# Kernel tuning notes

Measured on AMD Instinct MI355X. Metric: run time of the kernel, lower is better.

The kernel has to match this reference:

```python
import jax, jax.numpy as jnp
import numpy as np

B, LQ, H, NH, LK, N = 32, 256, 256, 8, 512, 8192
DH = H // NH
EPS = 1e-12

def layer_norm(x, g, b):
    m = x.mean(-1, keepdims=True)
    v = ((x - m) ** 2).mean(-1, keepdims=True)
    return (x - m) / jnp.sqrt(v + EPS) * g + b

def setup_inputs() -> dict:
    rs = np.random.RandomState(0)
    counts = rs.randint(LK // 2, LK + 1, size=B)  # ragged per-graph edge counts, max = LK
    E = int(counts.sum())
    edge_batch = jnp.asarray(np.repeat(np.arange(B), counts), jnp.int32)
    edge_pos = jnp.asarray(np.concatenate([np.arange(c) for c in counts]), jnp.int32)
    pad_mask = jnp.asarray((np.arange(LK)[None, :] < counts[:, None]).astype(np.float32))
    src = jnp.asarray(rs.randint(0, N, E), jnp.int32)
    dst = jnp.asarray(rs.randint(0, N, E), jnp.int32)
    ks = jax.random.split(jax.random.key(0), 16)
    def rn(i, shape, s=0.02):
        return jax.random.normal(ks[i], shape, jnp.float32) * s
    return dict(
        extended_attention_mask=jnp.zeros((B, 1, 1, LQ), jnp.float32),
        query=rn(0, (B, LQ, H), 1.0),
        rel_embedding_output=rn(1, (E, H), 1.0),
        graph_output=rn(2, (N, H), 1.0),
        src=src, dst=dst, edge_batch=edge_batch, edge_pos=edge_pos, pad_mask=pad_mask,
        Wq=rn(3, (H, H)), bq=jnp.zeros((H,), jnp.float32),
        Wk=rn(4, (2 * H, H)), bk=jnp.zeros((H,), jnp.float32),
        Wv=rn(5, (H, H)), bv=jnp.zeros((H,), jnp.float32),
        Wo=rn(6, (H, H)), bo=jnp.zeros((H,), jnp.float32),
        ln1_g=jnp.ones((H,), jnp.float32), ln1_b=jnp.zeros((H,), jnp.float32),
        W1=rn(7, (H, H)), b1=jnp.zeros((H,), jnp.float32),
        W2=rn(8, (H, H)), b2=jnp.zeros((H,), jnp.float32),
        ln2_g=jnp.ones((H,), jnp.float32), ln2_b=jnp.zeros((H,), jnp.float32),
    )

def reference(extended_attention_mask, query, rel_embedding_output, graph_output,
              src, dst, edge_batch, edge_pos, pad_mask,
              Wq, bq, Wk, bk, Wv, bv, Wo, bo, ln1_g, ln1_b,
              W1, b1, W2, b2, ln2_g, ln2_b):
    # --- memory_transform: edge gather + ragged pad (vectorized scatter) ---
    key_flat = jnp.concatenate([graph_output[src], rel_embedding_output], -1)  # [E, 2H]
    dst_flat = graph_output[dst]                                               # [E, H]
    key_pad = jnp.zeros((B, LK, 2 * H), key_flat.dtype).at[edge_batch, edge_pos].set(key_flat)
    val_pad = jnp.zeros((B, LK, H), dst_flat.dtype).at[edge_batch, edge_pos].set(dst_flat)
    cross_mask = (1.0 - pad_mask)[:, None, None, :] * -10000.0                 # [B,1,1,LK]
    # --- BidiAttention ---
    Q = (query @ Wq + bq).reshape(B, LQ, NH, DH)
    K = (key_pad @ Wk + bk).reshape(B, LK, NH, DH)
    V = (val_pad @ Wv + bv).reshape(B, LK, NH, DH)
    scores = jnp.einsum('bqhd,bkhd->bhqk', Q, K) / np.float32(np.sqrt(DH))
    pq = jax.nn.softmax(scores + cross_mask, axis=-1)
    query_ctx = jnp.einsum('bhqk,bkhd->bqhd', pq, V).reshape(B, LQ, H)
    pv = jax.nn.softmax(scores.transpose(0, 1, 3, 2) + extended_attention_mask, axis=-1)
    value_ctx = jnp.einsum('bhkq,bqhd->bkhd', pv, Q).reshape(B, LK, H)
    # --- RelAwareCross output / gate ---
    query_out = layer_norm(query_ctx @ Wo + bo + query, ln1_g, ln1_b)
    theta = jax.nn.sigmoid(value_ctx @ W1 + b1 + val_pad @ W2 + b2)
    value_new = layer_norm(theta * value_ctx + (1.0 - theta) * val_pad, ln2_g, ln2_b)
    # --- memory_update: unpad + scatter-mean by dst, replace rows with incoming edges ---
    val_edges = value_new[edge_batch, edge_pos]                                # [E, H]
    sums = jax.ops.segment_sum(val_edges, dst, num_segments=N)
    cnts = jax.ops.segment_sum(jnp.ones((val_edges.shape[0],), val_edges.dtype), dst, num_segments=N)
    mean = sums / jnp.maximum(cnts, 1.0)[:, None]
    graph_new = jnp.where((cnts > 0)[:, None], mean, graph_output)
    return (graph_new, query_out)
```

## Files before the change

### kernel.cpp

```cpp
#include <hip/hip_runtime.h>
#include <hip/hip_bf16.h>
#include <string.h>

#define B_ 32
#define LQ_ 256
#define H_ 256
#define NH_ 8
#define LK_ 512
#define N_ 8192
#define DH_ 32

typedef float floatx4 __attribute__((ext_vector_type(4)));
typedef short shortx8 __attribute__((ext_vector_type(8)));
typedef short shortx4 __attribute__((ext_vector_type(4)));

__device__ __forceinline__ short f2b(float f) {
    __hip_bfloat16 h = __float2bfloat16(f);
    short s;
    __builtin_memcpy(&s, &h, 2);
    return s;
}
__device__ __forceinline__ float b2f(short s) {
    unsigned u = ((unsigned)(unsigned short)s) << 16;
    float f;
    __builtin_memcpy(&f, &u, 4);
    return f;
}

#define LOG2E 1.44269504088896f

__global__ __launch_bounds__(256) void phase1(
    const float* __restrict__ graph, const float* __restrict__ rel,
    const int* __restrict__ src, const int* __restrict__ dst,
    const int* __restrict__ eb, const int* __restrict__ ep,
    const float* __restrict__ pad_mask,
    const float* __restrict__ Wq, const float* __restrict__ Wk,
    const float* __restrict__ Wv, const float* __restrict__ Wo,
    const float* __restrict__ W1, const float* __restrict__ W2,
    short* __restrict__ WT, short* __restrict__ key_pad,
    short* __restrict__ val_pad, int* __restrict__ head,
    int* __restrict__ row2e, int E) {
    const int bid = blockIdx.x, tid = threadIdx.x;
    if (bid < 8192) {
        int row = bid * 2 + (tid >> 7);
        int t = tid & 127;
        int b = row >> 9, p = row & 511;
        bool valid = pad_mask[row] > 0.5f;
        size_t krow = (size_t)row * 512;
        size_t vrow = (size_t)row * 256;
        int kc = t * 4, vc = t * 2;
        if (valid) {
            int lo = 0, hi = E;
            while (lo < hi) { int mid = (lo + hi) >> 1; if (eb[mid] < b) lo = mid + 1; else hi = mid; }
            int e = lo + p;
            int s = src[e], d = dst[e];
            const float* sp = (kc < 256) ? (graph + (size_t)s * 256 + kc)
                                         : (rel + (size_t)e * 256 + (kc - 256));
            float4 k4 = *(const float4*)sp;
            key_pad[krow + kc + 0] = f2b(k4.x);
            key_pad[krow + kc + 1] = f2b(k4.y);
            key_pad[krow + kc + 2] = f2b(k4.z);
            key_pad[krow + kc + 3] = f2b(k4.w);
            float2 v2 = *(const float2*)(graph + (size_t)d * 256 + vc);
            val_pad[vrow + vc + 0] = f2b(v2.x);
            val_pad[vrow + vc + 1] = f2b(v2.y);
        } else {
            *(long long*)&key_pad[krow + kc] = 0;
            *(int*)&val_pad[vrow + vc] = 0;
        }
    } else if (bid < 9984) {
        int i = (bid - 8192) * 256 + tid;
        const float* s;
        int K, loc;
        if (i < 65536) { s = Wq; K = 256; loc = i; }
        else if (i < 196608) { s = Wk; K = 512; loc = i - 65536; }
        else {
            int m = (i - 196608) >> 16;
            loc = (i - 196608) & 65535;
            K = 256;
            s = (m == 0) ? Wv : (m == 1) ? Wo : (m == 2) ? W1 : W2;
        }
        int n = loc / K, k = loc - n * K;
        WT[i] = f2b(s[(size_t)k * 256 + n]);
    } else {
        int i = (bid - 9984) * 256 + tid;
        if (i < 8192) head[i] = -1;
        for (int j = i; j < E; j += 8192)
            row2e[eb[j] * 512 + ep[j]] = j;
    }
}

__global__ __launch_bounds__(256) void phase2_gemm(
    const float* __restrict__ query, const short* __restrict__ key_pad,
    const short* __restrict__ val_pad, const short* __restrict__ WT,
    const float* __restrict__ bq, const float* __restrict__ bk,
    const float* __restrict__ bv,
    short* __restrict__ Qb, short* __restrict__ Kb,
    short* __restrict__ Vt, short* __restrict__ Qt) {
    __shared__ short As[128][40];
    __shared__ short Bs[128][40];
    const int tid = threadIdx.x;
    const int id = blockIdx.x;
    const float* Af = nullptr; const short* Ab = nullptr;
    const float* Bf = nullptr; const short* Bb = nullptr;
    const float* bias; short* C;
    size_t cbase; int cstride, K; bool biasM;
    if (id < 128) {
        int mt = id >> 1, nt = id & 1;
        Af = query + (size_t)(mt * 128) * 256; K = 256;
        Bb = WT + (size_t)(nt * 128) * 256;
        bias = bq + nt * 128; biasM = false;
        C = Qb; cbase = (size_t)(mt * 128) * 256 + nt * 128; cstride = 256;
    } else if (id < 384) {
        int t = id - 128; int mt = t >> 1, nt = t & 1;
        Ab = key_pad + (size_t)(mt * 128) * 512; K = 512;
        Bb = WT + 65536 + (size_t)(nt * 128) * 512;
        bias = bk + nt * 128; biasM = false;
        C = Kb; cbase = (size_t)(mt * 128) * 256 + nt * 128; cstride = 256;
    } else if (id < 640) {
        int t = id - 384; int b = t >> 3, ct = (t >> 2) & 1, nt = t & 3;
        Ab = WT + 196608 + (size_t)(ct * 128) * 256; K = 256;
        Bb = val_pad + ((size_t)(b * 512 + nt * 128)) * 256;
        bias = bv + ct * 128; biasM = true;
        C = Vt; cbase = ((size_t)(b * 256 + ct * 128)) * 512 + nt * 128; cstride = 512;
    } else {
        int t = id - 640; int b = t >> 2, ct = (t >> 1) & 1, qt = t & 1;
        Ab = WT + (size_t)(ct * 128) * 256; K = 256;
        Bf = query + ((size_t)(b * 256 + qt * 128)) * 256;
        bias = bq + ct * 128; biasM = true;
        C = Qt; cbase = ((size_t)(b * 256 + ct * 128)) * 256 + qt * 128; cstride = 256;
    }
    const int w = tid >> 6, lane = tid & 63;
    const int R0 = (w >> 1) * 64, C0 = (w & 1) * 64;
    const int lm = lane & 15, quad = lane >> 4;
    const int sr = tid >> 1, skq = (tid & 1) * 16;

    floatx4 acc[4][4];
#pragma unroll
    for (int i = 0; i < 4; i++)
#pragma unroll
        for (int j = 0; j < 4; j++) acc[i][j] = {0.f, 0.f, 0.f, 0.f};

    for (int kc = 0; kc < K; kc += 32) {
        if (Af) {
            const float* ap = Af + (size_t)sr * K + kc + skq;
            float4 a1 = *(const float4*)ap, a2 = *(const float4*)(ap + 4);
            float4 a3 = *(const float4*)(ap + 8), a4 = *(const float4*)(ap + 12);
            As[sr][skq + 0] = f2b(a1.x); As[sr][skq + 1] = f2b(a1.y);
            As[sr][skq + 2] = f2b(a1.z); As[sr][skq + 3] = f2b(a1.w);
            As[sr][skq + 4] = f2b(a2.x); As[sr][skq + 5] = f2b(a2.y);
            As[sr][skq + 6] = f2b(a2.z); As[sr][skq + 7] = f2b(a2.w);
            As[sr][skq + 8] = f2b(a3.x); As[sr][skq + 9] = f2b(a3.y);
            As[sr][skq + 10] = f2b(a3.z); As[sr][skq + 11] = f2b(a3.w);
            As[sr][skq + 12] = f2b(a4.x); As[sr][skq + 13] = f2b(a4.y);
            As[sr][skq + 14] = f2b(a4.z); As[sr][skq + 15] = f2b(a4.w);
        } else {
            const short* ap = Ab + (size_t)sr * K + kc + skq;
            *(shortx8*)&As[sr][skq] = *(const shortx8*)ap;
            *(shortx8*)&As[sr][skq + 8] = *(const shortx8*)(ap + 8);
        }
        if (Bf) {
            const float* bp = Bf + (size_t)sr * K + kc + skq;
            float4 a1 = *(const float4*)bp, a2 = *(const float4*)(bp + 4);
            float4 a3 = *(const float4*)(bp + 8), a4 = *(const float4*)(bp + 12);
            Bs[sr][skq + 0] = f2b(a1.x); Bs[sr][skq + 1] = f2b(a1.y);
            Bs[sr][skq + 2] = f2b(a1.z); Bs[sr][skq + 3] = f2b(a1.w);
            Bs[sr][skq + 4] = f2b(a2.x); Bs[sr][skq + 5] = f2b(a2.y);
            Bs[sr][skq + 6] = f2b(a2.z); Bs[sr][skq + 7] = f2b(a2.w);
            Bs[sr][skq + 8] = f2b(a3.x); Bs[sr][skq + 9] = f2b(a3.y);
            Bs[sr][skq + 10] = f2b(a3.z); Bs[sr][skq + 11] = f2b(a3.w);
            Bs[sr][skq + 12] = f2b(a4.x); Bs[sr][skq + 13] = f2b(a4.y);
            Bs[sr][skq + 14] = f2b(a4.z); Bs[sr][skq + 15] = f2b(a4.w);
        } else {
            const short* bp = Bb + (size_t)sr * K + kc + skq;
            *(shortx8*)&Bs[sr][skq] = *(const shortx8*)bp;
            *(shortx8*)&Bs[sr][skq + 8] = *(const shortx8*)(bp + 8);
        }
        __syncthreads();
        shortx8 af[4], bf[4];
#pragma unroll
        for (int i = 0; i < 4; i++) {
            af[i] = *(const shortx8*)&As[R0 + i * 16 + lm][quad * 8];
            bf[i] = *(const shortx8*)&Bs[C0 + i * 16 + lm][quad * 8];
        }
#pragma unroll
        for (int i = 0; i < 4; i++)
#pragma unroll
            for (int j = 0; j < 4; j++)
                acc[i][j] = __builtin_amdgcn_mfma_f32_16x16x32_bf16(af[i], bf[j], acc[i][j], 0, 0, 0);
        __syncthreads();
    }
#pragma unroll
    for (int i = 0; i < 4; i++) {
#pragma unroll
        for (int j = 0; j < 4; j++) {
            int gn = C0 + j * 16 + lm;
#pragma unroll
            for (int r = 0; r < 4; r++) {
                int gm = R0 + i * 16 + quad * 4 + r;
                float bvv = biasM ? bias[gm] : bias[gn];
                C[cbase + (size_t)gm * cstride + gn] = f2b(acc[i][j][r] + bvv);
            }
        }
    }
}

__global__ __launch_bounds__(512, 4) void phase3_attn(
    const short* __restrict__ Qm, const short* __restrict__ Km,
    const short* __restrict__ Vt, const short* __restrict__ Qt,
    const float* __restrict__ pad_mask, const float* __restrict__ ext,
    short* __restrict__ qctx, short* __restrict__ vctx) {
    __shared__ short SA[128][40];
    __shared__ short ST[32][136];
    __shared__ short P[8][32][72];
    const int tid = threadIdx.x;
    const int w = tid >> 6, lane = tid & 63;
    const int lm = lane & 15, quad = lane >> 4;
    const float scale2 = 0.17677669529663687f * LOG2E;
    const int id = blockIdx.x;
    short (*Pw)[72] = P[w];

    if (id < 256) {
        const int b = id >> 3, h = id & 7;
        shortx8 bqf[2];
        bqf[0] = *(const shortx8*)(Qm + ((size_t)(b * 256 + w * 32 + lm)) * 256 + h * 32 + quad * 8);
        bqf[1] = *(const shortx8*)(Qm + ((size_t)(b * 256 + w * 32 + 16 + lm)) * 256 + h * 32 + quad * 8);
        floatx4 oacc[2][2] = {{{0.f,0.f,0.f,0.f},{0.f,0.f,0.f,0.f}},
                              {{0.f,0.f,0.f,0.f},{0.f,0.f,0.f,0.f}}};
        float psum[2] = {0.f, 0.f};
        const floatx4* pmp = (const floatx4*)(pad_mask + b * 512);
        for (int kc = 0; kc < 512; kc += 128) {
            if (tid < 256) {
                int r = tid >> 1, dq = (tid & 1) * 16;
                const short* kp = Km + ((size_t)(b * 512 + kc + r)) * 256 + h * 32 + dq;
                *(shortx8*)&SA[r][dq] = *(const shortx8*)kp;
                *(shortx8*)&SA[r][dq + 8] = *(const shortx8*)(kp + 8);
            } else {
                int u = tid - 256;
                int r = u >> 3, kq = (u & 7) * 16;
                const short* vp = Vt + ((size_t)(b * 256 + h * 32 + r)) * 512 + kc + kq;
                *(shortx8*)&ST[r][kq] = *(const shortx8*)vp;
                *(shortx8*)&ST[r][kq + 8] = *(const shortx8*)(vp + 8);
            }
            __syncthreads();
#pragma unroll
            for (int kh = 0; kh < 2; kh++) {
#pragma unroll
                for (int kt = 0; kt < 4; kt++) {
                    shortx8 ak = *(const shortx8*)&SA[kh * 64 + kt * 16 + lm][quad * 8];
                    floatx4 pm = pmp[kc / 4 + kh * 16 + kt * 4 + quad];
#pragma unroll
                    for (int qf = 0; qf < 2; qf++) {
                        floatx4 s = {0.f, 0.f, 0.f, 0.f};
                        s = __builtin_amdgcn_mfma_f32_16x16x32_bf16(ak, bqf[qf], s, 0, 0, 0);
                        shortx4 p4;
#pragma unroll
                        for (int r = 0; r < 4; r++) {
                            float e = __builtin_amdgcn_exp2f(
                                s[r] * scale2 + (1.0f - pm[r]) * (-10000.0f * LOG2E));
                            psum[qf] += e;
                            p4[r] = f2b(e);
                        }
                        *(long long*)&Pw[qf * 16 + lm][kt * 16 + quad * 4] = *(long long*)&p4;
                    }
                }
#pragma unroll
                for (int ks = 0; ks < 2; ks++) {
#pragma unroll
                    for (int qf = 0; qf < 2; qf++) {
                        shortx8 pb = *(const shortx8*)&Pw[qf * 16 + lm][ks * 32 + quad * 8];
#pragma unroll
                        for (int di = 0; di < 2; di++) {
                            shortx8 av = *(const shortx8*)&ST[di * 16 + lm][kh * 64 + ks * 32 + quad * 8];
                            oacc[qf][di] = __builtin_amdgcn_mfma_f32_16x16x32_bf16(av, pb, oacc[qf][di], 0, 0, 0);
                        }
                    }
                }
            }
            __syncthreads();
        }
#pragma unroll
        for (int qf = 0; qf < 2; qf++) {
            psum[qf] += __shfl_xor(psum[qf], 16, 64);
            psum[qf] += __shfl_xor(psum[qf], 32, 64);
            float inv = 1.0f / psum[qf];
            int q = w * 32 + qf * 16 + lm;
            short* op = qctx + ((size_t)(b * 256 + q)) * 256 + h * 32;
#pragma unroll
            for (int di = 0; di < 2; di++) {
                shortx4 o;
#pragma unroll
                for (int r = 0; r < 4; r++) o[r] = f2b(oacc[qf][di][r] * inv);
                *(long long*)(op + di * 16 + quad * 4) = *(long long*)&o;
            }
        }
    } else {
        const int t = id - 256;
        const int b = t >> 4, h = (t >> 1) & 7, khb = t & 1;
        shortx8 bkf[2];
        bkf[0] = *(const shortx8*)(Km + ((size_t)(b * 512 + khb * 256 + w * 32 + lm)) * 256 + h * 32 + quad * 8);
        bkf[1] = *(const shortx8*)(Km + ((size_t)(b * 512 + khb * 256 + w * 32 + 16 + lm)) * 256 + h * 32 + quad * 8);
        floatx4 oacc[2][2] = {{{0.f,0.f,0.f,0.f},{0.f,0.f,0.f,0.f}},
                              {{0.f,0.f,0.f,0.f},{0.f,0.f,0.f,0.f}}};
        float psum[2] = {0.f, 0.f};
        const floatx4* emp = (const floatx4*)(ext + b * 256);
        for (int qc = 0; qc < 256; qc += 128) {
            if (tid < 256) {
                int r = tid >> 1, dq = (tid & 1) * 16;
                const short* qp = Qm + ((size_t)(b * 256 + qc + r)) * 256 + h * 32 + dq;
                *(shortx8*)&SA[r][dq] = *(const shortx8*)qp;
                *(shortx8*)&SA[r][dq + 8] = *(const shortx8*)(qp + 8);
            } else {
                int u = tid - 256;
                int r = u >> 3, kq = (u & 7) * 16;
                const short* tp = Qt + ((size_t)(b * 256 + h * 32 + r)) * 256 + qc + kq;
                *(shortx8*)&ST[r][kq] = *(const shortx8*)tp;
                *(shortx8*)&ST[r][kq + 8] = *(const shortx8*)(tp + 8);
            }
            __syncthreads();
#pragma unroll
            for (int qh = 0; qh < 2; qh++) {
#pragma unroll
                for (int qt = 0; qt < 4; qt++) {
                    shortx8 aq = *(const shortx8*)&SA[qh * 64 + qt * 16 + lm][quad * 8];
                    floatx4 em = emp[qc / 4 + qh * 16 + qt * 4 + quad];
#pragma unroll
                    for (int kf = 0; kf < 2; kf++) {
                        floatx4 s = {0.f, 0.f, 0.f, 0.f};
                        s = __builtin_amdgcn_mfma_f32_16x16x32_bf16(aq, bkf[kf], s, 0, 0, 0);
                        shortx4 p4;
#pragma unroll
                        for (int r = 0; r < 4; r++) {
                            float e = __builtin_amdgcn_exp2f(s[r] * scale2 + em[r] * LOG2E);
                            psum[kf] += e;
                            p4[r] = f2b(e);
                        }
                        *(long long*)&Pw[kf * 16 + lm][qt * 16 + quad * 4] = *(long long*)&p4;
                    }
                }
#pragma unroll
                for (int ks = 0; ks < 2; ks++) {
#pragma unroll
                    for (int kf = 0; kf < 2; kf++) {
                        shortx8 pb = *(const shortx8*)&Pw[kf * 16 + lm][ks * 32 + quad * 8];
#pragma unroll
                        for (int di = 0; di < 2; di++) {
                            shortx8 aT = *(const shortx8*)&ST[di * 16 + lm][qh * 64 + ks * 32 + quad * 8];
                            oacc[kf][di] = __builtin_amdgcn_mfma_f32_16x16x32_bf16(aT, pb, oacc[kf][di], 0, 0, 0);
                        }
                    }
                }
            }
            __syncthreads();
        }
#pragma unroll
        for (int kf = 0; kf < 2; kf++) {
            psum[kf] += __shfl_xor(psum[kf], 16, 64);
            psum[kf] += __shfl_xor(psum[kf], 32, 64);
            float inv = 1.0f / psum[kf];
            int k = khb * 256 + w * 32 + kf * 16 + lm;
            short* op = vctx + ((size_t)(b * 512 + k)) * 256 + h * 32;
#pragma unroll
            for (int di = 0; di < 2; di++) {
                shortx4 o;
#pragma unroll
                for (int r = 0; r < 4; r++) o[r] = f2b(oacc[kf][di][r] * inv);
                *(long long*)(op + di * 16 + quad * 4) = *(long long*)&o;
            }
        }
    }
}

__global__ __launch_bounds__(256) void phase4a_gemm(
    const short* __restrict__ qctx, const short* __restrict__ vctx,
    const short* __restrict__ val_pad, const short* __restrict__ WTo,
    const short* __restrict__ WT1, const short* __restrict__ WT2,
    float* __restrict__ obuf, float* __restrict__ tbuf) {
    __shared__ short As[128][40];
    __shared__ short Bs[128][40];
    const int tid = threadIdx.x;
    const int id = blockIdx.x;
    const bool is_out = id < 128;
    int t = is_out ? id : id - 128;
    const int mt = t >> 1, nt = t & 1;
    const int w = tid >> 6, lane = tid & 63;
    const int R0 = (w >> 1) * 64, C0 = (w & 1) * 64;
    const int lm = lane & 15, quad = lane >> 4;
    const int sr = tid >> 1, skq = (tid & 1) * 16;
    const int npair = is_out ? 1 : 2;

    floatx4 acc[4][4];
#pragma unroll
    for (int i = 0; i < 4; i++)
#pragma unroll
        for (int j = 0; j < 4; j++) acc[i][j] = {0.f, 0.f, 0.f, 0.f};

    for (int pair = 0; pair < npair; pair++) {
        const short* Ap = is_out ? (qctx + (size_t)(mt * 128) * 256)
                                 : (pair == 0 ? vctx + (size_t)(mt * 128) * 256
                                              : val_pad + (size_t)(mt * 128) * 256);
        const short* Bp = is_out ? (WTo + (size_t)(nt * 128) * 256)
                                 : (pair == 0 ? WT1 + (size_t)(nt * 128) * 256
                                              : WT2 + (size_t)(nt * 128) * 256);
        for (int kc = 0; kc < 256; kc += 32) {
            const short* ap = Ap + (size_t)sr * 256 + kc + skq;
            *(shortx8*)&As[sr][skq] = *(const shortx8*)ap;
            *(shortx8*)&As[sr][skq + 8] = *(const shortx8*)(ap + 8);
            const short* bp = Bp + (size_t)sr * 256 + kc + skq;
            *(shortx8*)&Bs[sr][skq] = *(const shortx8*)bp;
            *(shortx8*)&Bs[sr][skq + 8] = *(const shortx8*)(bp + 8);
            __syncthreads();
            shortx8 af[4], bf[4];
#pragma unroll
            for (int i = 0; i < 4; i++) {
                af[i] = *(const shortx8*)&As[R0 + i * 16 + lm][quad * 8];
                bf[i] = *(const shortx8*)&Bs[C0 + i * 16 + lm][quad * 8];
            }
#pragma unroll
            for (int i = 0; i < 4; i++)
#pragma unroll
                for (int j = 0; j < 4; j++)
                    acc[i][j] = __builtin_amdgcn_mfma_f32_16x16x32_bf16(af[i], bf[j], acc[i][j], 0, 0, 0);
            __syncthreads();
        }
    }
    float* C = is_out ? obuf : tbuf;
    const size_t cbase = (size_t)(mt * 128) * 256 + nt * 128;
#pragma unroll
    for (int i = 0; i < 4; i++) {
#pragma unroll
        for (int j = 0; j < 4; j++) {
            int gn = C0 + j * 16 + lm;
#pragma unroll
            for (int r = 0; r < 4; r++) {
                int gm = R0 + i * 16 + quad * 4 + r;
                C[cbase + (size_t)gm * 256 + gn] = acc[i][j][r];
            }
        }
    }
}

__global__ __launch_bounds__(256) void phase4b_ln(
    const float* __restrict__ obuf, const float* __restrict__ bo,
    const float* __restrict__ query, const float* __restrict__ g1,
    const float* __restrict__ be1, float* __restrict__ out_q,
    float* __restrict__ tbuf, const short* __restrict__ vctx,
    const short* __restrict__ val_pad, const float* __restrict__ b1_,
    const float* __restrict__ b2_, const float* __restrict__ g2,
    const float* __restrict__ be2, const float* __restrict__ pad_mask,
    const int* __restrict__ row2e, const int* __restrict__ dst,
    int* __restrict__ head, int* __restrict__ nxt) {
    const int lane = threadIdx.x & 63, w = threadIdx.x >> 6;
    const int c0 = lane * 4;
    if (blockIdx.x < 2048) {
        int row = blockIdx.x * 4 + w;
        long long base = (long long)row * H_ + c0;
        float4 o = *(const float4*)(obuf + base);
        float4 bo4 = *(const float4*)(bo + c0);
        float4 q4 = *(const float4*)(query + base);
        float x0 = o.x + bo4.x + q4.x, x1 = o.y + bo4.y + q4.y;
        float x2 = o.z + bo4.z + q4.z, x3 = o.w + bo4.w + q4.w;
        float t = x0 + x1 + x2 + x3;
        for (int off = 32; off > 0; off >>= 1) t += __shfl_xor(t, off, 64);
        float mean = t * (1.0f / H_);
        float d0 = x0 - mean, d1 = x1 - mean, d2 = x2 - mean, d3 = x3 - mean;
        float v = d0 * d0 + d1 * d1 + d2 * d2 + d3 * d3;
        for (int off = 32; off > 0; off >>= 1) v += __shfl_xor(v, off, 64);
        float rs = rsqrtf(v * (1.0f / H_) + 1e-12f);
        float4 g = *(const float4*)(g1 + c0);
        float4 be = *(const float4*)(be1 + c0);
        float4 out;
        out.x = d0 * rs * g.x + be.x; out.y = d1 * rs * g.y + be.y;
        out.z = d2 * rs * g.z + be.z; out.w = d3 * rs * g.w + be.w;
        *(float4*)(out_q + base) = out;
    } else {
        int row = (blockIdx.x - 2048) * 4 + w;
        if (pad_mask[row] > 0.5f) {
            long long base = (long long)row * H_ + c0;
            float4 tb = *(const float4*)(tbuf + base);
            float4 b14 = *(const float4*)(b1_ + c0);
            float4 b24 = *(const float4*)(b2_ + c0);
            shortx4 vc = *(const shortx4*)(vctx + base);
            shortx4 vp = *(const shortx4*)(val_pad + base);
            float x[4];
#pragma unroll
            for (int j = 0; j < 4; j++) {
                float tv = (j == 0) ? tb.x : (j == 1) ? tb.y : (j == 2) ? tb.z : tb.w;
                float bb1 = (j == 0) ? b14.x : (j == 1) ? b14.y : (j == 2) ? b14.z : b14.w;
                float bb2 = (j == 0) ? b24.x : (j == 1) ? b24.y : (j == 2) ? b24.z : b24.w;
                float th = 1.0f / (1.0f + __expf(-(tv + bb1 + bb2)));
                x[j] = th * b2f(vc[j]) + (1.0f - th) * b2f(vp[j]);
            }
            float t = x[0] + x[1] + x[2] + x[3];
            for (int off = 32; off > 0; off >>= 1) t += __shfl_xor(t, off, 64);
            float mean = t * (1.0f / H_);
            float d0 = x[0] - mean, d1 = x[1] - mean, d2 = x[2] - mean, d3 = x[3] - mean;
            float v = d0 * d0 + d1 * d1 + d2 * d2 + d3 * d3;
            for (int off = 32; off > 0; off >>= 1) v += __shfl_xor(v, off, 64);
            float rs = rsqrtf(v * (1.0f / H_) + 1e-12f);
            float4 g = *(const float4*)(g2 + c0);
            float4 be = *(const float4*)(be2 + c0);
            float4 y4;
            y4.x = d0 * rs * g.x + be.x; y4.y = d1 * rs * g.y + be.y;
            y4.z = d2 * rs * g.z + be.z; y4.w = d3 * rs * g.w + be.w;
            *(float4*)(tbuf + base) = y4;
            if (lane == 0) {
                int d = dst[row2e[row]];
                int prev = atomicExch(&head[d], row);
                nxt[row] = prev;
            }
        }
    }
}

__global__ __launch_bounds__(256) void finalize_graph(
    const int* __restrict__ head, const int* __restrict__ nxt,
    const float* __restrict__ yrows, const float* __restrict__ graph,
    float* __restrict__ out_g) {
    int n = blockIdx.x, c = threadIdx.x;
    long long idx = (long long)n * H_ + c;
    int e = head[n];
    if (e < 0) { out_g[idx] = graph[idx]; return; }
    float acc = 0.f;
    int cnt = 0;
    while (e >= 0) {
        acc += yrows[(size_t)e * H_ + c];
        cnt++;
        e = nxt[e];
    }
    out_g[idx] = acc / (float)cnt;
}

extern "C" void kernel_launch(void* const* d_in, const int* in_sizes, int n_in,
                              void* d_out, int out_size, void* d_ws, size_t ws_size,
                              hipStream_t stream) {
    const float* ext_mask = (const float*)d_in[0];
    const float* query    = (const float*)d_in[1];
    const float* rel      = (const float*)d_in[2];
    const float* graph    = (const float*)d_in[3];
    const int*  src      = (const int*)d_in[4];
    const int*  dst      = (const int*)d_in[5];
    const int*  eb       = (const int*)d_in[6];
    const int*  ep       = (const int*)d_in[7];
    const float* pad_mask = (const float*)d_in[8];
    const float* Wq = (const float*)d_in[9];  const float* bq = (const float*)d_in[10];
    const float* Wk = (const float*)d_in[11]; const float* bk = (const float*)d_in[12];
    const float* Wv = (const float*)d_in[13]; const float* bv = (const float*)d_in[14];
    const float* Wo = (const float*)d_in[15]; const float* bo = (const float*)d_in[16];
    const float* g1 = (const float*)d_in[17]; const float* be1 = (const float*)d_in[18];
    const float* W1 = (const float*)d_in[19]; const float* b1 = (const float*)d_in[20];
    const float* W2 = (const float*)d_in[21]; const float* b2 = (const float*)d_in[22];
    const float* g2 = (const float*)d_in[23]; const float* be2 = (const float*)d_in[24];
    const int E = in_sizes[2] / H_;

    float* out_g = (float*)d_out;
    float* out_q = (float*)d_out + (size_t)N_ * H_;

    short* sp = (short*)d_ws;
    short* key_pad = sp; sp += (size_t)B_ * LK_ * 2 * H_;
    short* val_pad = sp; sp += (size_t)B_ * LK_ * H_;
    short* Qb      = sp; sp += (size_t)B_ * LQ_ * H_;
    short* Kb      = sp; sp += (size_t)B_ * LK_ * H_;
    short* Vt      = sp; sp += (size_t)B_ * H_ * LK_;
    short* Qt      = sp; sp += (size_t)B_ * H_ * LQ_;
    short* qctx    = sp; sp += (size_t)B_ * LQ_ * H_;
    short* vctx    = sp; sp += (size_t)B_ * LK_ * H_;
    short* WT      = sp; sp += 458752;
    short* WTo = WT + 262144;
    short* WT1 = WT + 327680;
    short* WT2 = WT + 393216;
    int* ip = (int*)(((size_t)sp + 15) & ~(size_t)15);
    int* head  = ip; ip += N_;
    int* nxt   = ip; ip += B_ * LK_;
    int* row2e = ip; ip += B_ * LK_;
    float* fp = (float*)ip;
    float* obuf = fp; fp += (size_t)B_ * LQ_ * H_;
    float* tbuf = fp; fp += (size_t)B_ * LK_ * H_;

    phase1<<<10016, 256, 0, stream>>>(graph, rel, src, dst, eb, ep, pad_mask,
                                      Wq, Wk, Wv, Wo, W1, W2,
                                      WT, key_pad, val_pad, head, row2e, E);
    phase2_gemm<<<768, 256, 0, stream>>>(query, key_pad, val_pad, WT,
                                         bq, bk, bv, Qb, Kb, Vt, Qt);
    phase3_attn<<<768, 512, 0, stream>>>(Qb, Kb, Vt, Qt, pad_mask, ext_mask,
                                         qctx, vctx);
    phase4a_gemm<<<384, 256, 0, stream>>>(qctx, vctx, val_pad, WTo, WT1, WT2,
                                          obuf, tbuf);
    phase4b_ln<<<6144, 256, 0, stream>>>(obuf, bo, query, g1, be1, out_q,
                                         tbuf, vctx, val_pad, b1, b2, g2, be2,
                                         pad_mask, row2e, dst, head, nxt);
    finalize_graph<<<N_, 256, 0, stream>>>(head, nxt, tbuf, graph, out_g);
}
```

Baseline: 237.5 us.

## Fuse output GEMMs with bias, gate and layernorm epilogue into one kernel

Merges the output-projection and gate GEMM kernel with the following layernorm kernel. Each block now computes full 64-row by 256-column tiles, so row statistics can be reduced in-block and the epilogue applied directly. This removes the fp32 intermediate buffer round-trip and one kernel launch. It also changes LDS padding in the attention kernel and raises its occupancy hint. The cost is fewer, larger tiles with more B-matrix staging per block, and uncoalesced strided reads of query, vctx and val_pad in the epilogue.

```diff
diff --git a/kernel.cpp b/kernel.cpp
--- a/kernel.cpp
+++ b/kernel.cpp
@@ -205,20 +205,20 @@
     }
 }
 
-__global__ __launch_bounds__(512, 4) void phase3_attn(
+__global__ __launch_bounds__(512, 6) void phase3_attn(
     const short* __restrict__ Qm, const short* __restrict__ Km,
     const short* __restrict__ Vt, const short* __restrict__ Qt,
     const float* __restrict__ pad_mask, const float* __restrict__ ext,
     short* __restrict__ qctx, short* __restrict__ vctx) {
-    __shared__ short SA[128][40];
-    __shared__ short ST[32][136];
-    __shared__ short P[8][32][72];
+    __shared__ short SA[128][36];
+    __shared__ short ST[32][132];
+    __shared__ short P[8][32][68];
     const int tid = threadIdx.x;
     const int w = tid >> 6, lane = tid & 63;
     const int lm = lane & 15, quad = lane >> 4;
     const float scale2 = 0.17677669529663687f * LOG2E;
     const int id = blockIdx.x;
-    short (*Pw)[72] = P[w];
+    short (*Pw)[68] = P[w];
 
     if (id < 256) {
         const int b = id >> 3, h = id & 7;
@@ -371,23 +371,35 @@
     }
 }
 
-__global__ __launch_bounds__(256) void phase4a_gemm(
+__global__ __launch_bounds__(256) void phase4_fused(
     const short* __restrict__ qctx, const short* __restrict__ vctx,
     const short* __restrict__ val_pad, const short* __restrict__ WTo,
     const short* __restrict__ WT1, const short* __restrict__ WT2,
-    float* __restrict__ obuf, float* __restrict__ tbuf) {
-    __shared__ short As[128][40];
-    __shared__ short Bs[128][40];
+    const float* __restrict__ query, const float* __restrict__ bo,
+    const float* __restrict__ g1, const float* __restrict__ be1,
+    const float* __restrict__ b1_, const float* __restrict__ b2_,
+    const float* __restrict__ g2, const float* __restrict__ be2,
+    const float* __restrict__ pad_mask, const int* __restrict__ row2e,
+    const int* __restrict__ dst, int* __restrict__ head, int* __restrict__ nxt,
+    float* __restrict__ out_q, float* __restrict__ tbuf) {
+    __shared__ short As[64][40];
+    __shared__ short Bs[256][40];
+    __shared__ float2 red[4][64];
     const int tid = threadIdx.x;
-    const int id = blockIdx.x;
-    const bool is_out = id < 128;
-    int t = is_out ? id : id - 128;
-    const int mt = t >> 1, nt = t & 1;
     const int w = tid >> 6, lane = tid & 63;
-    const int R0 = (w >> 1) * 64, C0 = (w & 1) * 64;
     const int lm = lane & 15, quad = lane >> 4;
-    const int sr = tid >> 1, skq = (tid & 1) * 16;
-    const int npair = is_out ? 1 : 2;
+    const int C0 = w * 64;
+    const bool isA = blockIdx.x < 128;
+    const int row0 = (isA ? (int)blockIdx.x : (int)blockIdx.x - 128) * 64;
+
+    if (!isA && tid < 64) {
+        int row = row0 + tid;
+        if (pad_mask[row] > 0.5f) {
+            int d = dst[row2e[row]];
+            int prev = atomicExch(&head[d], row);
+            nxt[row] = prev;
+        }
+    }
 
     floatx4 acc[4][4];
 #pragma unroll
@@ -395,25 +407,30 @@
 #pragma unroll
         for (int j = 0; j < 4; j++) acc[i][j] = {0.f, 0.f, 0.f, 0.f};
 
+    const int npair = isA ? 1 : 2;
     for (int pair = 0; pair < npair; pair++) {
-        const short* Ap = is_out ? (qctx + (size_t)(mt * 128) * 256)
-                                 : (pair == 0 ? vctx + (size_t)(mt * 128) * 256
-                                              : val_pad + (size_t)(mt * 128) * 256);
-        const short* Bp = is_out ? (WTo + (size_t)(nt * 128) * 256)
-                                 : (pair == 0 ? WT1 + (size_t)(nt * 128) * 256
-                                              : WT2 + (size_t)(nt * 128) * 256);
+        const short* Ap = isA ? (qctx + (size_t)row0 * 256)
+                              : ((pair == 0 ? vctx : val_pad) + (size_t)row0 * 256);
+        const short* Bp = isA ? WTo : (pair == 0 ? WT1 : WT2);
         for (int kc = 0; kc < 256; kc += 32) {
-            const short* ap = Ap + (size_t)sr * 256 + kc + skq;
-            *(shortx8*)&As[sr][skq] = *(const shortx8*)ap;
-            *(shortx8*)&As[sr][skq + 8] = *(const shortx8*)(ap + 8);
-            const short* bp = Bp + (size_t)sr * 256 + kc + skq;
-            *(shortx8*)&Bs[sr][skq] = *(const shortx8*)bp;
-            *(shortx8*)&Bs[sr][skq + 8] = *(const shortx8*)(bp + 8);
+            if (tid < 128) {
+                int r = tid >> 1, sq = (tid & 1) * 16;
+                const short* ap = Ap + (size_t)r * 256 + kc + sq;
+                *(shortx8*)&As[r][sq] = *(const shortx8*)ap;
+                *(shortx8*)&As[r][sq + 8] = *(const shortx8*)(ap + 8);
+            }
+            {
+                const short* bp = Bp + (size_t)tid * 256 + kc;
+                *(shortx8*)&Bs[tid][0] = *(const shortx8*)bp;
+                *(shortx8*)&Bs[tid][8] = *(const shortx8*)(bp + 8);
+                *(shortx8*)&Bs[tid][16] = *(const shortx8*)(bp + 16);
+                *(shortx8*)&Bs[tid][24] = *(const shortx8*)(bp + 24);
+            }
             __syncthreads();
             shortx8 af[4], bf[4];
 #pragma unroll
             for (int i = 0; i < 4; i++) {
-                af[i] = *(const shortx8*)&As[R0 + i * 16 + lm][quad * 8];
+                af[i] = *(const shortx8*)&As[i * 16 + lm][quad * 8];
                 bf[i] = *(const shortx8*)&Bs[C0 + i * 16 + lm][quad * 8];
             }
 #pragma unroll
@@ -424,8 +441,14 @@
             __syncthreads();
         }
     }
-    float* C = is_out ? obuf : tbuf;
-    const size_t cbase = (size_t)(mt * 128) * 256 + nt * 128;
+
+    float bb[4], gg[4], bee[4];
+#pragma unroll
+    for (int j = 0; j < 4; j++) {
+        int gn = C0 + j * 16 + lm;
+        if (isA) { bb[j] = bo[gn]; gg[j] = g1[gn]; bee[j] = be1[gn]; }
+        else     { bb[j] = b1_[gn] + b2_[gn]; gg[j] = g2[gn]; bee[j] = be2[gn]; }
+    }
 #pragma unroll
     for (int i = 0; i < 4; i++) {
 #pragma unroll
@@ -433,81 +456,55 @@
             int gn = C0 + j * 16 + lm;
 #pragma unroll
             for (int r = 0; r < 4; r++) {
-                int gm = R0 + i * 16 + quad * 4 + r;
-                C[cbase + (size_t)gm * 256 + gn] = acc[i][j][r];
-            }
-        }
-    }
-}
-
-__global__ __launch_bounds__(256) void phase4b_ln(
-    const float* __restrict__ obuf, const float* __restrict__ bo,
-    const float* __restrict__ query, const float* __restrict__ g1,
-    const float* __restrict__ be1, float* __restrict__ out_q,
-    float* __restrict__ tbuf, const short* __restrict__ vctx,
-    const short* __restrict__ val_pad, const float* __restrict__ b1_,
-    const float* __restrict__ b2_, const float* __restrict__ g2,
-    const float* __restrict__ be2, const float* __restrict__ pad_mask,
-    const int* __restrict__ row2e, const int* __restrict__ dst,
-    int* __restrict__ head, int* __restrict__ nxt) {
-    const int lane = threadIdx.x & 63, w = threadIdx.x >> 6;
-    const int c0 = lane * 4;
-    if (blockIdx.x < 2048) {
-        int row = blockIdx.x * 4 + w;
-        long long base = (long long)row * H_ + c0;
-        float4 o = *(const float4*)(obuf + base);
-        float4 bo4 = *(const float4*)(bo + c0);
-        float4 q4 = *(const float4*)(query + base);
-        float x0 = o.x + bo4.x + q4.x, x1 = o.y + bo4.y + q4.y;
-        float x2 = o.z + bo4.z + q4.z, x3 = o.w + bo4.w + q4.w;
-        float t = x0 + x1 + x2 + x3;
-        for (int off = 32; off > 0; off >>= 1) t += __shfl_xor(t, off, 64);
-        float mean = t * (1.0f / H_);
-        float d0 = x0 - mean, d1 = x1 - mean, d2 = x2 - mean, d3 = x3 - mean;
-        float v = d0 * d0 + d1 * d1 + d2 * d2 + d3 * d3;
-        for (int off = 32; off > 0; off >>= 1) v += __shfl_xor(v, off, 64);
-        float rs = rsqrtf(v * (1.0f / H_) + 1e-12f);
-        float4 g = *(const float4*)(g1 + c0);
-        float4 be = *(const float4*)(be1 + c0);
-        float4 out;
-        out.x = d0 * rs * g.x + be.x; out.y = d1 * rs * g.y + be.y;
-        out.z = d2 * rs * g.z + be.z; out.w = d3 * rs * g.w + be.w;
-        *(float4*)(out_q + base) = out;
-    } else {
-        int row = (blockIdx.x - 2048) * 4 + w;
-        if (pad_mask[row] > 0.5f) {
-            long long base = (long long)row * H_ + c0;
-            float4 tb = *(const float4*)(tbuf + base);
-            float4 b14 = *(const float4*)(b1_ + c0);
-            float4 b24 = *(const float4*)(b2_ + c0);
-            shortx4 vc = *(const shortx4*)(vctx + base);
-            shortx4 vp = *(const shortx4*)(val_pad + base);
-            float x[4];
+                int gm = i * 16 + quad * 4 + r;
+                size_t idx = (size_t)(row0 + gm) * 256 + gn;
+                if (isA) {
+                    acc[i][j][r] += bb[j] + query[idx];
+                } else {
+                    float th = 1.0f / (1.0f + __expf(-(acc[i][j][r] + bb[j])));
+                    acc[i][j][r] = th * b2f(vctx[idx]) + (1.0f - th) * b2f(val_pad[idx]);
+                }
+            }
+        }
+    }
+#pragma unroll
+    for (int i = 0; i < 4; i++) {
+#pragma unroll
+        for (int r = 0; r < 4; r++) {
+            float s = 0.f, s2 = 0.f;
 #pragma unroll
             for (int j = 0; j < 4; j++) {
-                float tv = (j == 0) ? tb.x : (j == 1) ? tb.y : (j == 2) ? tb.z : tb.w;
-                float bb1 = (j == 0) ? b14.x : (j == 1) ? b14.y : (j == 2) ? b14.z : b14.w;
-                float bb2 = (j == 0) ? b24.x : (j == 1) ? b24.y : (j == 2) ? b24.z : b24.w;
-                float th = 1.0f / (1.0f + __expf(-(tv + bb1 + bb2)));
-                x[j] = th * b2f(vc[j]) + (1.0f - th) * b2f(vp[j]);
-            }
-            float t = x[0] + x[1] + x[2] + x[3];
-            for (int off = 32; off > 0; off >>= 1) t += __shfl_xor(t, off, 64);
-            float mean = t * (1.0f / H_);
-            float d0 = x[0] - mean, d1 = x[1] - mean, d2 = x[2] - mean, d3 = x[3] - mean;
-            float v = d0 * d0 + d1 * d1 + d2 * d2 + d3 * d3;
-            for (int off = 32; off > 0; off >>= 1) v += __shfl_xor(v, off, 64);
-            float rs = rsqrtf(v * (1.0f / H_) + 1e-12f);
-            float4 g = *(const float4*)(g2 + c0);
-            float4 be = *(const float4*)(be2 + c0);
-            float4 y4;
-            y4.x = d0 * rs * g.x + be.x; y4.y = d1 * rs * g.y + be.y;
-            y4.z = d2 * rs * g.z + be.z; y4.w = d3 * rs * g.w + be.w;
-            *(float4*)(tbuf + base) = y4;
-            if (lane == 0) {
-                int d = dst[row2e[row]];
-                int prev = atomicExch(&head[d], row);
-                nxt[row] = prev;
+                float v = acc[i][j][r];
+                s += v; s2 += v * v;
+            }
+            s += __shfl_xor(s, 1, 64);  s2 += __shfl_xor(s2, 1, 64);
+            s += __shfl_xor(s, 2, 64);  s2 += __shfl_xor(s2, 2, 64);
+            s += __shfl_xor(s, 4, 64);  s2 += __shfl_xor(s2, 4, 64);
+            s += __shfl_xor(s, 8, 64);  s2 += __shfl_xor(s2, 8, 64);
+            if (lm == 0) red[w][i * 16 + quad * 4 + r] = make_float2(s, s2);
+        }
+    }
+    __syncthreads();
+    float* Out = isA ? out_q : tbuf;
+#pragma unroll
+    for (int i = 0; i < 4; i++) {
+#pragma unroll
+        for (int r = 0; r < 4; r++) {
+            int row = i * 16 + quad * 4 + r;
+            float S = 0.f, S2 = 0.f;
+#pragma unroll
+            for (int ww = 0; ww < 4; ww++) {
+                float2 t = red[ww][row];
+                S += t.x; S2 += t.y;
+            }
+            float mean = S * (1.0f / H_);
+            float var = S2 * (1.0f / H_) - mean * mean;
+            float rsv = rsqrtf(var + 1e-12f);
+#pragma unroll
+            for (int j = 0; j < 4; j++) {
+                int gn = C0 + j * 16 + lm;
+                Out[(size_t)(row0 + row) * 256 + gn] =
+                    (acc[i][j][r] - mean) * rsv * gg[j] + bee[j];
             }
         }
     }
@@ -574,7 +571,6 @@
     int* nxt   = ip; ip += B_ * LK_;
     int* row2e = ip; ip += B_ * LK_;
     float* fp = (float*)ip;
-    float* obuf = fp; fp += (size_t)B_ * LQ_ * H_;
     float* tbuf = fp; fp += (size_t)B_ * LK_ * H_;
 
     phase1<<<10016, 256, 0, stream>>>(graph, rel, src, dst, eb, ep, pad_mask,
@@ -584,10 +580,9 @@
                                          bq, bk, bv, Qb, Kb, Vt, Qt);
     phase3_attn<<<768, 512, 0, stream>>>(Qb, Kb, Vt, Qt, pad_mask, ext_mask,
                                          qctx, vctx);
-    phase4a_gemm<<<384, 256, 0, stream>>>(qctx, vctx, val_pad, WTo, WT1, WT2,
-                                          obuf, tbuf);
-    phase4b_ln<<<6144, 256, 0, stream>>>(obuf, bo, query, g1, be1, out_q,
-                                         tbuf, vctx, val_pad, b1, b2, g2, be2,
-                                         pad_mask, row2e, dst, head, nxt);
+    phase4_fused<<<384, 256, 0, stream>>>(qctx, vctx, val_pad, WTo, WT1, WT2,
+                                          query, bo, g1, be1, b1, b2, g2, be2,
+                                          pad_mask, row2e, dst, head, nxt,
+                                          out_q, tbuf);
     finalize_graph<<<N_, 256, 0, stream>>>(head, nxt, tbuf, graph, out_g);
 }
```

Result: slower. 258.9 us (+9.0%).
